# Kernel tuning notes

Measured on AMD Instinct MI355X. Metric: run time of the kernel, lower is better.

The kernel has to match this reference:

```python
import jax, jax.numpy as jnp
import numpy as np
import math

N, E, C, H = 16384, 8192, 256, 8
NNZ = 262144  # incidence pairs, avg vertex degree 16


def setup_inputs() -> dict:
    key = jax.random.key(0)
    ks = jax.random.split(key, 12)
    s = 1.0 / math.sqrt(C)
    inp = {
        "X": jax.random.normal(ks[0], (N, C), dtype=jnp.float32),
        "v_ids": jax.random.randint(ks[1], (NNZ,), 0, N, dtype=jnp.int32),
        "e_ids": jax.random.randint(ks[2], (NNZ,), 0, E, dtype=jnp.int32),
        # Linear params stored as [in, out]; y = x @ W + b  (matches torch x @ W.T + b)
        "Wq": jax.random.uniform(ks[3], (C, C), jnp.float32, -s, s),
        "bq": jax.random.uniform(ks[4], (C,), jnp.float32, -s, s),
        "Wk": jax.random.uniform(ks[5], (C, C), jnp.float32, -s, s),
        "bk": jax.random.uniform(ks[6], (C,), jnp.float32, -s, s),
        "Wv": jax.random.uniform(ks[7], (C, C), jnp.float32, -s, s),
        "bv": jax.random.uniform(ks[8], (C,), jnp.float32, -s, s),
        "Wke": jax.random.uniform(ks[9], (C, C), jnp.float32, -s, s),
        "bke": jax.random.uniform(ks[10], (C,), jnp.float32, -s, s),
    }
    return inp


def reference(X, v_ids, e_ids, Wq, bq, Wk, bk, Wv, bv, Wke, bke):
    d = C // H
    scale = 1.0 / math.sqrt(d)

    Q = (X @ Wq + bq).reshape(N, H, d)
    K = (X @ Wk + bk).reshape(N, H, d)
    V = (X @ Wv + bv).reshape(N, H, d)

    # hg.v2e_aggregation(X, 'mean'): segment-mean of incident vertex features per hyperedge
    sums = jax.ops.segment_sum(X[v_ids], e_ids, num_segments=E)          # [E, C]
    cnt = jax.ops.segment_sum(jnp.ones((NNZ,), X.dtype), e_ids, num_segments=E)
    Xe = sums / jnp.maximum(cnt, 1.0)[:, None]                            # [E, C]

    Ke = Xe @ Wke + bke                                                   # [E, C]
    Qe = X @ Wq + bq                                                      # [N, C]

    # per-node attention over heads: [N, H, H]
    attn_n = jax.nn.softmax(jnp.einsum('nhd,ngd->nhg', Q, K) * scale, axis=-1)
    X_node = jnp.einsum('nhg,ngd->nhd', attn_n, V).reshape(N, C)          # [N, C]

    # node -> hyperedge attention: [N, E]
    attn_e = jax.nn.softmax((Qe @ Ke.T) * scale, axis=-1)
    X_hyperedge = attn_e @ Xe                                             # [N, C]

    out = X_node + X_hyperedge
    # is_last=False: ReLU; bn=None; dropout in eval mode (identity)
    return jax.nn.relu(out)
```

## Files before the change

### kernel.cpp

```cpp
#include <hip/hip_runtime.h>

typedef unsigned short u16;
typedef unsigned int u32;
typedef __attribute__((ext_vector_type(4))) float f32x4;
typedef __attribute__((ext_vector_type(16))) float f32x16;
typedef __attribute__((ext_vector_type(8))) short bf16x8;
typedef __attribute__((ext_vector_type(4))) short bf16x4;
typedef __attribute__((ext_vector_type(4))) u16 u16x4;

#define N_NODES 16384
#define N_EDGES 8192
#define FK_SCALE 0.17677669529663687f
#define LOG2E 1.4426950408889634f
#define C1EXP (FK_SCALE * LOG2E)

typedef const u32 __attribute__((address_space(1))) gu32;
typedef u32 __attribute__((address_space(3))) lu32;

__device__ __forceinline__ void gl_lds16(const void* g, void* l) {
  __builtin_amdgcn_global_load_lds((gu32*)g, (lu32*)l, 16, 0, 0);
}

__device__ __forceinline__ float b2f(u16 u) {
  return __builtin_bit_cast(float, (u32)u << 16);
}
__device__ __forceinline__ u16 f2b(float f) {
  u32 u = __builtin_bit_cast(u32, f);
  u += 0x7fffu + ((u >> 16) & 1u);
  return (u16)(u >> 16);
}

__global__ __launch_bounds__(256) void k_prep(const float* __restrict__ X,
                                              const int* __restrict__ e_ids,
                                              u16* __restrict__ Xb,
                                              int* __restrict__ hist,
                                              const float* __restrict__ Wq,
                                              const float* __restrict__ Wk,
                                              const float* __restrict__ Wv,
                                              const float* __restrict__ Wke,
                                              const float* __restrict__ bq,
                                              const float* __restrict__ bk,
                                              const float* __restrict__ bv,
                                              const float* __restrict__ bke,
                                              u16* __restrict__ Wt,
                                              float* __restrict__ bcat) {
  __shared__ float tile[64][65];
  int b = blockIdx.x;
  int tid = threadIdx.x;
  if (b < 4096) {
    int i = b * 256 + tid;
    f32x4 v = *(const f32x4*)(X + (size_t)i * 4);
    u16x4 r;
    r.x = f2b(v.x); r.y = f2b(v.y); r.z = f2b(v.z); r.w = f2b(v.w);
    *(u16x4*)(Xb + (size_t)i * 4) = r;
    if (tid < 64) atomicAdd(&hist[e_ids[b * 64 + tid]], 1);
    return;
  }
  int local = b - 4096;
  int w = local >> 4, rem = local & 15;
  int k0 = (rem >> 2) * 64, n0 = (rem & 3) * 64;
  const float* W = (w == 0) ? Wq : (w == 1) ? Wk : (w == 2) ? Wv : Wke;
  if (rem == 0) {
    const float* bb = (w == 0) ? bq : (w == 1) ? bk : (w == 2) ? bv : bke;
    bcat[w * 256 + tid] = bb[tid];
  }
#pragma unroll
  for (int i = 0; i < 16; i++) {
    int idx = i * 256 + tid;
    int kr = idx >> 6, nc = idx & 63;
    tile[nc][kr] = W[(k0 + kr) * 256 + n0 + nc];
  }
  __syncthreads();
#pragma unroll
  for (int i = 0; i < 16; i++) {
    int idx = i * 256 + tid;
    int nr = idx >> 6, kc = idx & 63;
    Wt[w * 65536 + (n0 + nr) * 256 + k0 + kc] = f2b(tile[nr][kc]);
  }
}

__global__ __launch_bounds__(256) void k_scan(const int* __restrict__ hist,
                                              int* __restrict__ eoff,
                                              int* __restrict__ cur) {
  __shared__ int ts[256];
  int t = threadIdx.x;
  int base = t * 32;
  int vals[32];
  int s = 0;
#pragma unroll
  for (int i = 0; i < 32; i++) { vals[i] = hist[base + i]; s += vals[i]; }
  ts[t] = s;
  __syncthreads();
  for (int off = 1; off < 256; off <<= 1) {
    int v = (t >= off) ? ts[t - off] : 0;
    __syncthreads();
    ts[t] += v;
    __syncthreads();
  }
  int ex = ts[t] - s;
#pragma unroll
  for (int i = 0; i < 32; i++) {
    eoff[base + i] = ex;
    cur[base + i] = ex;
    ex += vals[i];
  }
  if (t == 255) eoff[8192] = ex;
}

__global__ __launch_bounds__(256) void k_perm(const int* __restrict__ v_ids,
                                              const int* __restrict__ e_ids,
                                              int* __restrict__ cur,
                                              int* __restrict__ perm) {
  int base = blockIdx.x * 1024 + threadIdx.x;
#pragma unroll
  for (int k = 0; k < 4; k++) {
    int i = base + k * 256;
    int e = e_ids[i];
    int v = v_ids[i];
    int pos = atomicAdd(&cur[e], 1);
    perm[pos] = v;
  }
}

__global__ __launch_bounds__(256) void k_gg(const u16* __restrict__ Xb,
                                            const int* __restrict__ perm,
                                            const int* __restrict__ eoff,
                                            u16* __restrict__ Xe,
                                            u16* __restrict__ XeTc,
                                            const u16* __restrict__ Wt,
                                            const float* __restrict__ bcat,
                                            u16* __restrict__ QKV) {
  __shared__ u16 As[128 * 64];
  __shared__ u16 Bs[128 * 64];
  int b = blockIdx.x;
  int tid = threadIdx.x;
  int wave = tid >> 6, lane = tid & 63;
  if (b < 768) {
    int quad = lane >> 4, l16 = lane & 15;
    int wm = wave >> 1, wn = wave & 1;
    int mtile = (b & 127) * 128, ntile = (b >> 7) * 128;
    const u16* Ap = Xb + (size_t)mtile * 256;
    const u16* Bp = Wt + (size_t)ntile * 256;
    f32x4 acc[4][4];
#pragma unroll
    for (int am = 0; am < 4; am++)
#pragma unroll
      for (int bn = 0; bn < 4; bn++) acc[am][bn] = (f32x4){0.f, 0.f, 0.f, 0.f};
    for (int ks = 0; ks < 4; ks++) {
      __syncthreads();
#pragma unroll
      for (int i = 0; i < 4; i++) {
        int s = i * 256 + tid;
        int r = s >> 3, c = s & 7;
        gl_lds16(Ap + r * 256 + ks * 64 + ((c ^ (r & 7)) << 3), As + s * 8);
      }
#pragma unroll
      for (int i = 0; i < 4; i++) {
        int s = i * 256 + tid;
        int r = s >> 3, c = s & 7;
        gl_lds16(Bp + r * 256 + ks * 64 + ((c ^ (r & 7)) << 3), Bs + s * 8);
      }
      __syncthreads();
#pragma unroll
      for (int kc = 0; kc < 2; kc++) {
        bf16x8 a[4], bb[4];
        int cc = kc * 4 + quad;
#pragma unroll
        for (int am = 0; am < 4; am++) {
          int rl = wm * 64 + am * 16 + l16;
          a[am] = *(const bf16x8*)(As + rl * 64 + ((cc ^ (rl & 7)) << 3));
        }
#pragma unroll
        for (int bn = 0; bn < 4; bn++) {
          int rl = wn * 64 + bn * 16 + l16;
          bb[bn] = *(const bf16x8*)(Bs + rl * 64 + ((cc ^ (rl & 7)) << 3));
        }
#pragma unroll
        for (int am = 0; am < 4; am++)
#pragma unroll
          for (int bn = 0; bn < 4; bn++)
            acc[am][bn] = __builtin_amdgcn_mfma_f32_16x16x32_bf16(a[am], bb[bn], acc[am][bn], 0, 0, 0);
      }
    }
#pragma unroll
    for (int am = 0; am < 4; am++)
#pragma unroll
      for (int bn = 0; bn < 4; bn++)
#pragma unroll
        for (int r = 0; r < 4; r++) {
          int row = mtile + wm * 64 + am * 16 + quad * 4 + r;
          int col = ntile + wn * 64 + bn * 16 + l16;
          QKV[(size_t)row * 768 + col] = f2b(acc[am][bn][r] + bcat[col]);
        }
    return;
  }
  int e = (b - 768) * 4 + wave;
  int start = eoff[e], end = eoff[e + 1];
  int cnt = end - start;
  int pidx = 0;
  if (lane < cnt) pidx = perm[start + lane];
  f32x4 acc = {0.f, 0.f, 0.f, 0.f};
  int n1 = cnt < 64 ? cnt : 64;
  for (int j = 0; j < n1; j++) {
    int v = __shfl(pidx, j, 64);
    bf16x4 x = *(const bf16x4*)(Xb + (size_t)v * 256 + lane * 4);
#pragma unroll
    for (int c = 0; c < 4; c++) acc[c] += b2f((u16)x[c]);
  }
  for (int j = start + 64; j < end; j++) {
    int v = perm[j];
    bf16x4 x = *(const bf16x4*)(Xb + (size_t)v * 256 + lane * 4);
#pragma unroll
    for (int c = 0; c < 4; c++) acc[c] += b2f((u16)x[c]);
  }
  float inv = 1.0f / fmaxf((float)cnt, 1.0f);
  u16x4 r;
  r.x = f2b(acc.x * inv); r.y = f2b(acc.y * inv);
  r.z = f2b(acc.z * inv); r.w = f2b(acc.w * inv);
  *(u16x4*)(Xe + (size_t)e * 256 + lane * 4) = r;
  size_t tb = (size_t)(e >> 3) * 2048 + (e & 7);
  XeTc[tb + (lane * 4 + 0) * 8] = r.x;
  XeTc[tb + (lane * 4 + 1) * 8] = r.y;
  XeTc[tb + (lane * 4 + 2) * 8] = r.z;
  XeTc[tb + (lane * 4 + 3) * 8] = r.w;
}

__global__ __launch_bounds__(256) void k_gemmke(const u16* __restrict__ A,
                                                const u16* __restrict__ Wt,
                                                const float* __restrict__ bias,
                                                u16* __restrict__ KebT) {
  __shared__ u16 As[128 * 64];
  __shared__ u16 Bs[128 * 64];
  int tid = threadIdx.x;
  int wave = tid >> 6, lane = tid & 63;
  int quad = lane >> 4, l16 = lane & 15;
  int wm = wave >> 1, wn = wave & 1;
  int mtile = blockIdx.x * 128, ntile = blockIdx.y * 128;
  const u16* Ap = A + (size_t)mtile * 256;
  const u16* Bp = Wt + (size_t)ntile * 256;
  f32x4 acc[4][4];
#pragma unroll
  for (int am = 0; am < 4; am++)
#pragma unroll
    for (int bn = 0; bn < 4; bn++) acc[am][bn] = (f32x4){0.f, 0.f, 0.f, 0.f};
  for (int ks = 0; ks < 4; ks++) {
    __syncthreads();
#pragma unroll
    for (int i = 0; i < 4; i++) {
      int s = i * 256 + tid;
      int r = s >> 3, c = s & 7;
      gl_lds16(Ap + r * 256 + ks * 64 + ((c ^ (r & 7)) << 3), As + s * 8);
    }
#pragma unroll
    for (int i = 0; i < 4; i++) {
      int s = i * 256 + tid;
      int r = s >> 3, c = s & 7;
      gl_lds16(Bp + r * 256 + ks * 64 + ((c ^ (r & 7)) << 3), Bs + s * 8);
    }
    __syncthreads();
#pragma unroll
    for (int kc = 0; kc < 2; kc++) {
      bf16x8 a[4], b[4];
      int cc = kc * 4 + quad;
#pragma unroll
      for (int am = 0; am < 4; am++) {
        int rl = wm * 64 + am * 16 + l16;
        a[am] = *(const bf16x8*)(As + rl * 64 + ((cc ^ (rl & 7)) << 3));
      }
#pragma unroll
      for (int bn = 0; bn < 4; bn++) {
        int rl = wn * 64 + bn * 16 + l16;
        b[bn] = *(const bf16x8*)(Bs + rl * 64 + ((cc ^ (rl & 7)) << 3));
      }
#pragma unroll
      for (int am = 0; am < 4; am++)
#pragma unroll
        for (int bn = 0; bn < 4; bn++)
          acc[am][bn] = __builtin_amdgcn_mfma_f32_16x16x32_bf16(a[am], b[bn], acc[am][bn], 0, 0, 0);
    }
  }
#pragma unroll
  for (int am = 0; am < 4; am++)
#pragma unroll
    for (int bn = 0; bn < 4; bn++)
#pragma unroll
      for (int r = 0; r < 4; r++) {
        int row = mtile + wm * 64 + am * 16 + quad * 4 + r;
        int col = ntile + wn * 64 + bn * 16 + l16;
        KebT[(size_t)(col >> 3) * 65536 + row * 8 + (col & 7)] = f2b(acc[am][bn][r] + bias[col]);
      }
}

__device__ __forceinline__ void stage_k(const u16* __restrict__ KebT, u16* KeL,
                                        int kbase, int tid) {
#pragma unroll
  for (int i = 0; i < 8; i++) {
    int s = i * 256 + tid;
    int c = s >> 6, r = s & 63;
    gl_lds16(KebT + ((size_t)c * 8192 + kbase + r) * 8, KeL + s * 8);
  }
}
__device__ __forceinline__ void stage_v(const u16* __restrict__ XeTc, u16* VLT,
                                        int ktg, int tid) {
  int kb8 = ktg * 8;
#pragma unroll
  for (int i = 0; i < 8; i++) {
    int s = i * 256 + tid;
    int kc = s >> 8, ch = s & 255;
    gl_lds16(XeTc + ((size_t)(kb8 + kc) * 256 + ch) * 8, VLT + s * 8);
  }
}

__global__ __launch_bounds__(256, 2) void k_flash(const u16* __restrict__ QKV,
                                                  const u16* __restrict__ KebT,
                                                  const u16* __restrict__ XeTc,
                                                  u16* __restrict__ Op,
                                                  float* __restrict__ Lv) {
  extern __shared__ u16 sm[];
  u16* KeL = sm;
  u16* VLT = sm + 16384;
  u16* PL = sm + 32768;
  int tid = threadIdx.x;
  int wave = tid >> 6, lane = tid & 63;
  int l31 = lane & 31, half = lane >> 5;
  int pair = wave >> 1, kh = wave & 1;
  int qt = blockIdx.x & 255;
  int split = blockIdx.x >> 8;
  int rowp0 = qt * 64 + pair * 32;
  u16* PLp = PL + pair * 2048;

  bf16x8 qf[16];
#pragma unroll
  for (int ks = 0; ks < 16; ks++)
    qf[ks] = *(const bf16x8*)(QKV + (rowp0 + l31) * 768 + ks * 16 + half * 8);

  f32x16 o[4];
#pragma unroll
  for (int i = 0; i < 4; i++)
#pragma unroll
    for (int r = 0; r < 16; r++) o[i][r] = 0.f;
  float l[16];
#pragma unroll
  for (int r = 0; r < 16; r++) l[r] = 0.f;

  stage_k(KebT, KeL, (split * 64) * 64, tid);

  for (int ktl = 0; ktl < 64; ktl++) {
    int ktg = split * 64 + ktl;
    __syncthreads();
    stage_v(XeTc, VLT, ktg, tid);

    f32x16 sc0, sc1;
#pragma unroll
    for (int r = 0; r < 16; r++) { sc0[r] = 0.f; sc1[r] = 0.f; }
#pragma unroll
    for (int ks = 0; ks < 8; ks++) {
      int c0 = ks * 2 + half;
      int c1 = (ks + 8) * 2 + half;
      bf16x8 kb0 = *(const bf16x8*)(KeL + c0 * 512 + (kh * 32 + l31) * 8);
      bf16x8 kb1 = *(const bf16x8*)(KeL + c1 * 512 + (kh * 32 + l31) * 8);
      sc0 = __builtin_amdgcn_mfma_f32_32x32x16_bf16(qf[ks], kb0, sc0, 0, 0, 0);
      sc1 = __builtin_amdgcn_mfma_f32_32x32x16_bf16(qf[ks + 8], kb1, sc1, 0, 0, 0);
    }
#pragma unroll
    for (int reg = 0; reg < 16; reg++) {
      float pv = __builtin_amdgcn_exp2f((sc0[reg] + sc1[reg]) * C1EXP);
      l[reg] += pv;
      int row = (reg & 3) + 8 * (reg >> 2) + 4 * half;
      int col = kh * 32 + l31;
      PLp[row * 64 + (((col >> 3) ^ (row & 7)) << 3) + (col & 7)] = f2b(pv);
    }
    __syncthreads();
    if (ktl + 1 < 64) stage_k(KebT, KeL, (ktg + 1) * 64, tid);

    bf16x8 pf[4];
#pragma unroll
    for (int ks = 0; ks < 4; ks++) {
      int pc = ks * 2 + half;
      pf[ks] = *(const bf16x8*)(PLp + l31 * 64 + ((pc ^ (l31 & 7)) << 3));
    }
#pragma unroll
    for (int ct = 0; ct < 4; ct++) {
#pragma unroll
      for (int ks = 0; ks < 4; ks++) {
        int kc = ks * 2 + half;
        int ch = kh * 128 + ct * 32 + l31;
        bf16x8 vb = *(const bf16x8*)(VLT + kc * 2048 + ch * 8);
        o[ct] = __builtin_amdgcn_mfma_f32_32x32x16_bf16(pf[ks], vb, o[ct], 0, 0, 0);
      }
    }
  }

#pragma unroll
  for (int off = 1; off < 32; off <<= 1)
#pragma unroll
    for (int r = 0; r < 16; r++) l[r] += __shfl_xor(l[r], off, 64);
  if (l31 == 0) {
#pragma unroll
    for (int reg = 0; reg < 16; reg++) {
      int row = (reg & 3) + 8 * (reg >> 2) + 4 * half;
      Lv[(split * 2 + kh) * N_NODES + rowp0 + row] = l[reg];
    }
  }

  size_t obase = (size_t)split * N_NODES * 256;
#pragma unroll
  for (int ct = 0; ct < 4; ct++)
#pragma unroll
    for (int reg = 0; reg < 16; reg++) {
      int row = rowp0 + (reg & 3) + 8 * (reg >> 2) + 4 * half;
      int col = kh * 128 + ct * 32 + l31;
      Op[obase + (size_t)row * 256 + col] = f2b(o[ct][reg]);
    }
}

__global__ __launch_bounds__(256) void k_comb(const u16* __restrict__ QKV,
                                              const u16* __restrict__ Op,
                                              const float* __restrict__ Lv,
                                              float* __restrict__ out) {
  int idx = blockIdx.x * 256 + threadIdx.x;
  int n = idx >> 6, lane = idx & 63;
  int h = lane >> 3, g = lane & 7;
  const u16* base = QKV + n * 768;
  const bf16x8* qp = (const bf16x8*)(base + h * 32);
  const bf16x8* kp = (const bf16x8*)(base + 256 + g * 32);
  float s = 0.f;
#pragma unroll
  for (int t = 0; t < 4; t++) {
    bf16x8 qv = qp[t], kv = kp[t];
#pragma unroll
    for (int j = 0; j < 8; j++) s += b2f((u16)qv[j]) * b2f((u16)kv[j]);
  }
  s *= FK_SCALE;
  float mx = s;
#pragma unroll
  for (int off = 1; off < 8; off <<= 1) mx = fmaxf(mx, __shfl_xor(mx, off, 64));
  float p = __builtin_amdgcn_exp2f((s - mx) * LOG2E);
  float lsum = p;
#pragma unroll
  for (int off = 1; off < 8; off <<= 1) lsum += __shfl_xor(lsum, off, 64);
  float attn = p / lsum;
  float a4[4] = {0.f, 0.f, 0.f, 0.f};
#pragma unroll
  for (int g2 = 0; g2 < 8; g2++) {
    float a = __shfl(attn, (lane & 56) | g2, 64);
    bf16x4 vv = *(const bf16x4*)(base + 512 + g2 * 32 + g * 4);
#pragma unroll
    for (int j = 0; j < 4; j++) a4[j] += a * b2f((u16)vv[j]);
  }
  int c4 = lane * 4;
  float L = 0.f;
#pragma unroll
  for (int sl = 0; sl < 4; sl++) L += Lv[sl * N_NODES + n];
  f32x4 acc = {0.f, 0.f, 0.f, 0.f};
#pragma unroll
  for (int sp = 0; sp < 2; sp++) {
    u16x4 ov = *(const u16x4*)(Op + (size_t)sp * N_NODES * 256 + (size_t)n * 256 + c4);
    acc.x += b2f(ov.x);
    acc.y += b2f(ov.y);
    acc.z += b2f(ov.z);
    acc.w += b2f(ov.w);
  }
  float invL = 1.0f / L;
  f32x4 res;
  res.x = fmaxf(acc.x * invL + a4[0], 0.f);
  res.y = fmaxf(acc.y * invL + a4[1], 0.f);
  res.z = fmaxf(acc.z * invL + a4[2], 0.f);
  res.w = fmaxf(acc.w * invL + a4[3], 0.f);
  *(f32x4*)(out + (size_t)n * 256 + c4) = res;
}

extern "C" void kernel_launch(void* const* d_in, const int* in_sizes, int n_in,
                              void* d_out, int out_size, void* d_ws, size_t ws_size,
                              hipStream_t stream) {
  const float* X = (const float*)d_in[0];
  const int* v_ids = (const int*)d_in[1];
  const int* e_ids = (const int*)d_in[2];
  const float* Wq = (const float*)d_in[3];
  const float* bq = (const float*)d_in[4];
  const float* Wk = (const float*)d_in[5];
  const float* bk = (const float*)d_in[6];
  const float* Wv = (const float*)d_in[7];
  const float* bv = (const float*)d_in[8];
  const float* Wke = (const float*)d_in[9];
  const float* bke = (const float*)d_in[10];
  float* out = (float*)d_out;

  char* ws = (char*)d_ws;
  u16* Xb = (u16*)(ws);
  u16* QKV = (u16*)(ws + 8388608);
  u16* Wt = (u16*)(ws + 33554432);
  float* bcat = (float*)(ws + 34078720);
  int* hist = (int*)(ws + 34082816);
  int* eoff = (int*)(ws + 34115584);
  int* cur = (int*)(ws + 34152448);
  int* perm = (int*)(ws + 34185216);
  u16* Xe = (u16*)(ws + 35233792);
  u16* XeTc = (u16*)(ws + 39428096);
  u16* KebT = (u16*)(ws + 43622400);
  u16* Op = (u16*)(ws + 64593920);
  float* Lv = (float*)(ws + 98148352);

  hipMemsetAsync(hist, 0, 32768, stream);
  k_prep<<<4160, 256, 0, stream>>>(X, e_ids, Xb, hist, Wq, Wk, Wv, Wke,
                                   bq, bk, bv, bke, Wt, bcat);
  k_scan<<<1, 256, 0, stream>>>(hist, eoff, cur);
  k_perm<<<256, 256, 0, stream>>>(v_ids, e_ids, cur, perm);
  k_gg<<<2816, 256, 0, stream>>>(Xb, perm, eoff, Xe, XeTc, Wt, bcat, QKV);
  k_gemmke<<<dim3(64, 2), 256, 0, stream>>>(Xe, Wt + 3 * 65536, bcat + 768, KebT);
  hipFuncSetAttribute((const void*)k_flash, hipFuncAttributeMaxDynamicSharedMemorySize,
                      73728);
  k_flash<<<512, 256, 73728, stream>>>(QKV, KebT, XeTc, Op, Lv);
  k_comb<<<4096, 256, 0, stream>>>(QKV, Op, Lv, out);
}
```

Measured before the change: 342.9 us.

## Keep attention probabilities in registers via transposed QK and lane permute

The flash kernel now computes S^T (Ke as the A operand), packs the exponentials to bf16 with v_cvt_pk_bf16_f32, and uses permlane32 swaps to form the PV operand in registers. This drops the LDS round trip for P. Each wave now owns 32 full query rows across all 256 channels, with 128 rows per block and 4 key splits instead of 2. It also adds s_setprio around the MFMA bursts. The cost is twice as many output accumulators per wave, which raises register pressure, and twice as much partial output for the combine kernel to read and sum.

```diff
diff --git a/kernel.cpp b/kernel.cpp
--- a/kernel.cpp
+++ b/kernel.cpp
@@ -7,6 +7,7 @@
 typedef __attribute__((ext_vector_type(8))) short bf16x8;
 typedef __attribute__((ext_vector_type(4))) short bf16x4;
 typedef __attribute__((ext_vector_type(4))) u16 u16x4;
+typedef __attribute__((ext_vector_type(4))) u32 u32x4;
 
 #define N_NODES 16384
 #define N_EDGES 8192
@@ -28,6 +29,27 @@
   u32 u = __builtin_bit_cast(u32, f);
   u += 0x7fffu + ((u >> 16) & 1u);
   return (u16)(u >> 16);
+}
+
+__device__ __forceinline__ u32 cvtpk(float a, float b) {
+  u32 r;
+  asm("v_cvt_pk_bf16_f32 %0, %1, %2" : "=v"(r) : "v"(a), "v"(b));
+  return r;
+}
+
+__device__ __forceinline__ void swap32(u32& x, u32& y) {
+#if __has_builtin(__builtin_amdgcn_permlane32_swap)
+  auto r = __builtin_amdgcn_permlane32_swap(x, y, false, false);
+  x = (u32)r[0];
+  y = (u32)r[1];
+#else
+  u32 px = __shfl_xor(x, 32, 64), py = __shfl_xor(y, 32, 64);
+  bool hi = (threadIdx.x & 32) != 0;
+  u32 nx = hi ? x : py;
+  u32 ny = hi ? px : y;
+  x = nx;
+  y = ny;
+#endif
 }
 
 __global__ __launch_bounds__(256) void k_prep(const float* __restrict__ X,
@@ -311,6 +333,43 @@
   }
 }
 
+__device__ __forceinline__ void qk_chunk(const u16* KeL, const bf16x8* qf, int cb,
+                                         int l31, int half, float& lsum,
+                                         bf16x8& pfa, bf16x8& pfb) {
+  f32x16 sa, sb;
+#pragma unroll
+  for (int r = 0; r < 16; r++) { sa[r] = 0.f; sb[r] = 0.f; }
+  const u16* kp = KeL + (cb + l31) * 8 + half * 512;
+  __builtin_amdgcn_s_setprio(1);
+#pragma unroll
+  for (int ks = 0; ks < 8; ks++) {
+    bf16x8 ka = *(const bf16x8*)(kp + ks * 1024);
+    bf16x8 kb = *(const bf16x8*)(kp + ks * 1024 + 8192);
+    sa = __builtin_amdgcn_mfma_f32_32x32x16_bf16(ka, qf[ks], sa, 0, 0, 0);
+    sb = __builtin_amdgcn_mfma_f32_32x32x16_bf16(kb, qf[ks + 8], sb, 0, 0, 0);
+  }
+  __builtin_amdgcn_s_setprio(0);
+  float p[16];
+#pragma unroll
+  for (int r = 0; r < 16; r++) {
+    float v = __builtin_amdgcn_exp2f((sa[r] + sb[r]) * C1EXP);
+    lsum += v;
+    p[r] = v;
+  }
+  u32 a0 = cvtpk(p[0], p[1]), a1 = cvtpk(p[2], p[3]);
+  u32 b0 = cvtpk(p[4], p[5]), b1 = cvtpk(p[6], p[7]);
+  u32 c0 = cvtpk(p[8], p[9]), c1 = cvtpk(p[10], p[11]);
+  u32 d0 = cvtpk(p[12], p[13]), d1 = cvtpk(p[14], p[15]);
+  swap32(b0, a0);
+  swap32(b1, a1);
+  swap32(d0, c0);
+  swap32(d1, c1);
+  u32x4 w0 = {a0, a1, b0, b1};
+  u32x4 w1 = {c0, c1, d0, d1};
+  pfa = __builtin_bit_cast(bf16x8, w0);
+  pfb = __builtin_bit_cast(bf16x8, w1);
+}
+
 __global__ __launch_bounds__(256, 2) void k_flash(const u16* __restrict__ QKV,
                                                   const u16* __restrict__ KebT,
                                                   const u16* __restrict__ XeTc,
@@ -319,97 +378,62 @@
   extern __shared__ u16 sm[];
   u16* KeL = sm;
   u16* VLT = sm + 16384;
-  u16* PL = sm + 32768;
   int tid = threadIdx.x;
   int wave = tid >> 6, lane = tid & 63;
   int l31 = lane & 31, half = lane >> 5;
-  int pair = wave >> 1, kh = wave & 1;
-  int qt = blockIdx.x & 255;
-  int split = blockIdx.x >> 8;
-  int rowp0 = qt * 64 + pair * 32;
-  u16* PLp = PL + pair * 2048;
+  int qt = blockIdx.x & 127;
+  int split = blockIdx.x >> 7;
+  int rowq = qt * 128 + wave * 32 + l31;
 
   bf16x8 qf[16];
 #pragma unroll
   for (int ks = 0; ks < 16; ks++)
-    qf[ks] = *(const bf16x8*)(QKV + (rowp0 + l31) * 768 + ks * 16 + half * 8);
-
-  f32x16 o[4];
-#pragma unroll
-  for (int i = 0; i < 4; i++)
+    qf[ks] = *(const bf16x8*)(QKV + (size_t)rowq * 768 + ks * 16 + half * 8);
+
+  f32x16 o[8];
+#pragma unroll
+  for (int i = 0; i < 8; i++)
 #pragma unroll
     for (int r = 0; r < 16; r++) o[i][r] = 0.f;
-  float l[16];
-#pragma unroll
-  for (int r = 0; r < 16; r++) l[r] = 0.f;
-
-  stage_k(KebT, KeL, (split * 64) * 64, tid);
-
-  for (int ktl = 0; ktl < 64; ktl++) {
-    int ktg = split * 64 + ktl;
+  float lsum = 0.f;
+
+  stage_k(KebT, KeL, split * 2048, tid);
+
+  for (int ktl = 0; ktl < 32; ktl++) {
+    int ktg = split * 32 + ktl;
     __syncthreads();
     stage_v(XeTc, VLT, ktg, tid);
 
-    f32x16 sc0, sc1;
-#pragma unroll
-    for (int r = 0; r < 16; r++) { sc0[r] = 0.f; sc1[r] = 0.f; }
-#pragma unroll
-    for (int ks = 0; ks < 8; ks++) {
-      int c0 = ks * 2 + half;
-      int c1 = (ks + 8) * 2 + half;
-      bf16x8 kb0 = *(const bf16x8*)(KeL + c0 * 512 + (kh * 32 + l31) * 8);
-      bf16x8 kb1 = *(const bf16x8*)(KeL + c1 * 512 + (kh * 32 + l31) * 8);
-      sc0 = __builtin_amdgcn_mfma_f32_32x32x16_bf16(qf[ks], kb0, sc0, 0, 0, 0);
-      sc1 = __builtin_amdgcn_mfma_f32_32x32x16_bf16(qf[ks + 8], kb1, sc1, 0, 0, 0);
+    bf16x8 pf0, pf1, pf2, pf3;
+    qk_chunk(KeL, qf, 0, l31, half, lsum, pf0, pf1);
+    qk_chunk(KeL, qf, 32, l31, half, lsum, pf2, pf3);
+
+    __syncthreads();
+    if (ktl + 1 < 32) stage_k(KebT, KeL, (ktg + 1) * 64, tid);
+
+    const u16* vp = VLT + half * 2048 + l31 * 8;
+    __builtin_amdgcn_s_setprio(1);
+#pragma unroll
+    for (int ct = 0; ct < 8; ct++) {
+      const u16* vpc = vp + ct * 256;
+      o[ct] = __builtin_amdgcn_mfma_f32_32x32x16_bf16(pf0, *(const bf16x8*)(vpc), o[ct], 0, 0, 0);
+      o[ct] = __builtin_amdgcn_mfma_f32_32x32x16_bf16(pf1, *(const bf16x8*)(vpc + 4096), o[ct], 0, 0, 0);
+      o[ct] = __builtin_amdgcn_mfma_f32_32x32x16_bf16(pf2, *(const bf16x8*)(vpc + 8192), o[ct], 0, 0, 0);
+      o[ct] = __builtin_amdgcn_mfma_f32_32x32x16_bf16(pf3, *(const bf16x8*)(vpc + 12288), o[ct], 0, 0, 0);
     }
+    __builtin_amdgcn_s_setprio(0);
+  }
+
+  lsum += __shfl_xor(lsum, 32, 64);
+  if (lane < 32) Lv[split * N_NODES + qt * 128 + wave * 32 + l31] = lsum;
+
+  size_t obase = (size_t)split * N_NODES * 256;
+#pragma unroll
+  for (int ct = 0; ct < 8; ct++)
 #pragma unroll
     for (int reg = 0; reg < 16; reg++) {
-      float pv = __builtin_amdgcn_exp2f((sc0[reg] + sc1[reg]) * C1EXP);
-      l[reg] += pv;
-      int row = (reg & 3) + 8 * (reg >> 2) + 4 * half;
-      int col = kh * 32 + l31;
-      PLp[row * 64 + (((col >> 3) ^ (row & 7)) << 3) + (col & 7)] = f2b(pv);
-    }
-    __syncthreads();
-    if (ktl + 1 < 64) stage_k(KebT, KeL, (ktg + 1) * 64, tid);
-
-    bf16x8 pf[4];
-#pragma unroll
-    for (int ks = 0; ks < 4; ks++) {
-      int pc = ks * 2 + half;
-      pf[ks] = *(const bf16x8*)(PLp + l31 * 64 + ((pc ^ (l31 & 7)) << 3));
-    }
-#pragma unroll
-    for (int ct = 0; ct < 4; ct++) {
-#pragma unroll
-      for (int ks = 0; ks < 4; ks++) {
-        int kc = ks * 2 + half;
-        int ch = kh * 128 + ct * 32 + l31;
-        bf16x8 vb = *(const bf16x8*)(VLT + kc * 2048 + ch * 8);
-        o[ct] = __builtin_amdgcn_mfma_f32_32x32x16_bf16(pf[ks], vb, o[ct], 0, 0, 0);
-      }
-    }
-  }
-
-#pragma unroll
-  for (int off = 1; off < 32; off <<= 1)
-#pragma unroll
-    for (int r = 0; r < 16; r++) l[r] += __shfl_xor(l[r], off, 64);
-  if (l31 == 0) {
-#pragma unroll
-    for (int reg = 0; reg < 16; reg++) {
-      int row = (reg & 3) + 8 * (reg >> 2) + 4 * half;
-      Lv[(split * 2 + kh) * N_NODES + rowp0 + row] = l[reg];
-    }
-  }
-
-  size_t obase = (size_t)split * N_NODES * 256;
-#pragma unroll
-  for (int ct = 0; ct < 4; ct++)
-#pragma unroll
-    for (int reg = 0; reg < 16; reg++) {
-      int row = rowp0 + (reg & 3) + 8 * (reg >> 2) + 4 * half;
-      int col = kh * 128 + ct * 32 + l31;
+      int row = qt * 128 + wave * 32 + (reg & 3) + 8 * (reg >> 2) + 4 * half;
+      int col = ct * 32 + l31;
       Op[obase + (size_t)row * 256 + col] = f2b(o[ct][reg]);
     }
 }
@@ -454,7 +478,7 @@
   for (int sl = 0; sl < 4; sl++) L += Lv[sl * N_NODES + n];
   f32x4 acc = {0.f, 0.f, 0.f, 0.f};
 #pragma unroll
-  for (int sp = 0; sp < 2; sp++) {
+  for (int sp = 0; sp < 4; sp++) {
     u16x4 ov = *(const u16x4*)(Op + (size_t)sp * N_NODES * 256 + (size_t)n * 256 + c4);
     acc.x += b2f(ov.x);
     acc.y += b2f(ov.y);
@@ -509,7 +533,7 @@
   k_gg<<<2816, 256, 0, stream>>>(Xb, perm, eoff, Xe, XeTc, Wt, bcat, QKV);
   k_gemmke<<<dim3(64, 2), 256, 0, stream>>>(Xe, Wt + 3 * 65536, bcat + 768, KebT);
   hipFuncSetAttribute((const void*)k_flash, hipFuncAttributeMaxDynamicSharedMemorySize,
-                      73728);
-  k_flash<<<512, 256, 73728, stream>>>(QKV, KebT, XeTc, Op, Lv);
+                      65536);
+  k_flash<<<512, 256, 65536, stream>>>(QKV, KebT, XeTc, Op, Lv);
   k_comb<<<4096, 256, 0, stream>>>(QKV, Op, Lv, out);
 }
```

Measured after the change: 451.5 us. 31.7% more time.
